# Kernel optimization log

Measured on AMD Instinct MI355X. Metric: run time of the kernel, lower is better.

Reference implementation:

```python
import jax, jax.numpy as jnp
import numpy as np


def _bilinear_sample_zeros(img, px, py):
    """Bilinear sample img [B,C,H,W] at pixel coords px,py [B,...], zeros padding,
    align_corners=True semantics (coords are direct pixel indices)."""
    B, C, H, W = img.shape
    shp = px.shape
    px_f = px.reshape(B, -1)
    py_f = py.reshape(B, -1)
    x0 = jnp.floor(px_f)
    y0 = jnp.floor(py_f)
    fx = px_f - x0  # fractional offsets
    fy = py_f - y0
    x0i = x0.astype(jnp.int32)
    y0i = y0.astype(jnp.int32)
    img_flat = img.reshape(B, C, H * W)

    def corner(xi, yi, w):
        valid = ((xi >= 0) & (xi < W) & (yi >= 0) & (yi < H)).astype(img.dtype)
        xc = jnp.clip(xi, 0, W - 1)
        yc = jnp.clip(yi, 0, H - 1)
        idx = (yc * W + xc)[:, None, :]  # [B,1,N]
        v = jnp.take_along_axis(img_flat, idx, axis=2)  # [B,C,N]
        return v * (w * valid)[:, None, :]

    out = (corner(x0i, y0i, (1.0 - fx) * (1.0 - fy))
           + corner(x0i + 1, y0i, fx * (1.0 - fy))
           + corner(x0i, y0i + 1, (1.0 - fx) * fy)
           + corner(x0i + 1, y0i + 1, fx * fy))
    return out.reshape((B, C) + shp[1:])


def setup_inputs() -> dict:
    key = jax.random.key(0)
    k1, k2, k3 = jax.random.split(key, 3)
    B, C, H, W, D = 2, 32, 128, 256, 48
    x = jax.random.normal(k1, (B, C, H, W), dtype=jnp.float32)
    y = jax.random.normal(k2, (B, C, H, W), dtype=jnp.float32)
    disp = jax.random.uniform(k3, (B, D, H, W), dtype=jnp.float32) * 64.0
    return {"x": x, "y": y, "disp_range_samples": disp, "ndisp": D}


def reference(x, y, disp_range_samples, ndisp):
    B, C, H, W = x.shape
    # pixel coords of the warp: sample right image at (w - disparity, h)
    mw = jnp.arange(W, dtype=x.dtype).reshape(1, 1, 1, W)
    mh = jnp.arange(H, dtype=x.dtype).reshape(1, 1, H, 1)
    px = mw - disp_range_samples                       # [B, D, H, W]
    py = jnp.broadcast_to(mh, px.shape)                # [B, D, H, W]
    warped = _bilinear_sample_zeros(y, px, py)         # [B, C, D, H, W]
    # correlation mode: elementwise multiply with left features, mean over channels
    cost = (warped * x[:, :, None, :, :]).mean(axis=1)  # [B, D, H, W]
    return cost
```

## Files before the change

### kernel.cpp

```cpp
#include <hip/hip_runtime.h>

#define BB 2
#define CC 32
#define HH 128
#define WW 256
#define DD 48
#define HW (HH * WW)
#define NS 65
#define PAD 64
#define YROW (PAD + WW)
#define NT 512


__global__ __launch_bounds__(NT) void cost_volume_kernel(
    const float* __restrict__ x, const float* __restrict__ y,
    const float* __restrict__ disp, float* __restrict__ out) {
  __shared__ float xs[CC * WW];
  __shared__ float ys[CC * YROW];
  __shared__ float corr[NS * WW];

  const int bx = blockIdx.x;
  const int b = bx >> 7;
  const int h = bx & 127;
  const int tid = threadIdx.x;

  const int gbase = (b * CC * HH + h) * WW;
  {
    int c = tid >> 4;
    int j = (tid & 15) << 2;
    *(float4*)&ys[c * YROW + j] = make_float4(0.f, 0.f, 0.f, 0.f);
  }
#pragma unroll
  for (int k = 0; k < 4; ++k) {
    int t = tid + (k << 9);
    int c = t >> 6;
    int w = (t & 63) << 2;
    float4 vx = *(const float4*)(x + gbase + c * HW + w);
    float4 vy = *(const float4*)(y + gbase + c * HW + w);
    *(float4*)&xs[c * WW + w] = vx;
    *(float4*)&ys[c * YROW + PAD + w] = vy;
  }
  __syncthreads();

  const int wid = tid >> 6;
  const int lane = tid & 63;
  const int w0 = lane << 2;
  const int sbase = wid << 3;

  float acc[8][4];
#pragma unroll
  for (int sl = 0; sl < 8; ++sl)
#pragma unroll
    for (int wj = 0; wj < 4; ++wj) acc[sl][wj] = 0.f;
  float a64[4] = {0.f, 0.f, 0.f, 0.f};

  const int A = PAD + w0 - sbase - 8;
#pragma unroll 2
  for (int c = 0; c < CC; ++c) {
    const float* yrow = &ys[c * YROW];
    float4 xv = *(const float4*)&xs[c * WW + w0];
    float4 wv0 = *(const float4*)&yrow[A];
    float4 wv1 = *(const float4*)&yrow[A + 4];
    float4 wv2 = *(const float4*)&yrow[A + 8];
    float win[12] = {wv0.x, wv0.y, wv0.z, wv0.w, wv1.x, wv1.y,
                     wv1.z, wv1.w, wv2.x, wv2.y, wv2.z, wv2.w};
    float xr[4] = {xv.x, xv.y, xv.z, xv.w};
#pragma unroll
    for (int sl = 0; sl < 8; ++sl)
#pragma unroll
      for (int wj = 0; wj < 4; ++wj)
        acc[sl][wj] = fmaf(xr[wj], win[8 + wj - sl], acc[sl][wj]);
    if (wid == 7) {
      float4 yv = *(const float4*)&yrow[w0];
      a64[0] = fmaf(xr[0], yv.x, a64[0]);
      a64[1] = fmaf(xr[1], yv.y, a64[1]);
      a64[2] = fmaf(xr[2], yv.z, a64[2]);
      a64[3] = fmaf(xr[3], yv.w, a64[3]);
    }
  }
#pragma unroll
  for (int sl = 0; sl < 8; ++sl)
    *(float4*)&corr[(sbase + sl) * WW + w0] =
        make_float4(acc[sl][0], acc[sl][1], acc[sl][2], acc[sl][3]);
  if (wid == 7)
    *(float4*)&corr[64 * WW + w0] = make_float4(a64[0], a64[1], a64[2], a64[3]);
  __syncthreads();

  const float inv_c = 1.0f / (float)CC;
  const float* dbase = disp + (b * DD * HH + h) * WW;
  float* obase = out + (b * DD * HH + h) * WW;
#pragma unroll 4
  for (int k = 0; k < (DD * WW) / NT; ++k) {
    int idx = tid + (k << 9);
    int d = idx >> 8;
    int w = idx & 255;
    float dv = dbase[d * HW + w];
    float s0f = ceilf(dv);
    int i0 = (int)s0f;
    float fx = s0f - dv;
    int i1 = (i0 > 0) ? i0 - 1 : 0;
    float c0 = corr[i0 * WW + w];
    float c1 = corr[i1 * WW + w];
    obase[d * HW + w] = (c0 + fx * (c1 - c0)) * inv_c;
  }
}

extern "C" void kernel_launch(void* const* d_in, const int* in_sizes, int n_in,
                              void* d_out, int out_size, void* d_ws, size_t ws_size,
                              hipStream_t stream) {
  const float* x = (const float*)d_in[0];
  const float* y = (const float*)d_in[1];
  const float* disp = (const float*)d_in[2];
  float* out = (float*)d_out;
  cost_volume_kernel<<<BB * HH, NT, 0, stream>>>(x, y, disp, out);
}
```

Measured before the change: 89.55 us.

## Prefetch disparities early, read x directly from global, vectorize output stores

Drops the shared-memory staging of x and has each thread read its x float4 straight from global memory inside the channel loop. Disparity values are prefetched as float4 into registers before the first barrier so their latency overlaps the correlation compute. The output phase now writes float4 stores. This cuts LDS usage and memory stalls in exchange for more register pressure (24 extra floats held live) and global loads inside the hot loop.

```diff
diff --git a/kernel.cpp b/kernel.cpp
--- a/kernel.cpp
+++ b/kernel.cpp
@@ -15,7 +15,6 @@
 __global__ __launch_bounds__(NT) void cost_volume_kernel(
     const float* __restrict__ x, const float* __restrict__ y,
     const float* __restrict__ disp, float* __restrict__ out) {
-  __shared__ float xs[CC * WW];
   __shared__ float ys[CC * YROW];
   __shared__ float corr[NS * WW];
 
@@ -25,6 +24,7 @@
   const int tid = threadIdx.x;
 
   const int gbase = (b * CC * HH + h) * WW;
+
   {
     int c = tid >> 4;
     int j = (tid & 15) << 2;
@@ -35,10 +35,16 @@
     int t = tid + (k << 9);
     int c = t >> 6;
     int w = (t & 63) << 2;
-    float4 vx = *(const float4*)(x + gbase + c * HW + w);
-    float4 vy = *(const float4*)(y + gbase + c * HW + w);
-    *(float4*)&xs[c * WW + w] = vx;
-    *(float4*)&ys[c * YROW + PAD + w] = vy;
+    *(float4*)&ys[c * YROW + PAD + w] = *(const float4*)(y + gbase + c * HW + w);
+  }
+  const float* dbase = disp + (b * DD * HH + h) * WW;
+  float4 dv4[6];
+#pragma unroll
+  for (int j = 0; j < 6; ++j) {
+    int t = tid + (j << 9);
+    int d = t >> 6;
+    int w4 = (t & 63) << 2;
+    dv4[j] = *(const float4*)(dbase + d * HW + w4);
   }
   __syncthreads();
 
@@ -55,10 +61,11 @@
   float a64[4] = {0.f, 0.f, 0.f, 0.f};
 
   const int A = PAD + w0 - sbase - 8;
+  const float* xcol = x + gbase + w0;
 #pragma unroll 2
   for (int c = 0; c < CC; ++c) {
     const float* yrow = &ys[c * YROW];
-    float4 xv = *(const float4*)&xs[c * WW + w0];
+    float4 xv = *(const float4*)(xcol + c * HW);
     float4 wv0 = *(const float4*)&yrow[A];
     float4 wv1 = *(const float4*)&yrow[A + 4];
     float4 wv2 = *(const float4*)&yrow[A + 8];
@@ -87,21 +94,25 @@
   __syncthreads();
 
   const float inv_c = 1.0f / (float)CC;
-  const float* dbase = disp + (b * DD * HH + h) * WW;
   float* obase = out + (b * DD * HH + h) * WW;
-#pragma unroll 4
-  for (int k = 0; k < (DD * WW) / NT; ++k) {
-    int idx = tid + (k << 9);
-    int d = idx >> 8;
-    int w = idx & 255;
-    float dv = dbase[d * HW + w];
-    float s0f = ceilf(dv);
-    int i0 = (int)s0f;
-    float fx = s0f - dv;
-    int i1 = (i0 > 0) ? i0 - 1 : 0;
-    float c0 = corr[i0 * WW + w];
-    float c1 = corr[i1 * WW + w];
-    obase[d * HW + w] = (c0 + fx * (c1 - c0)) * inv_c;
+#pragma unroll
+  for (int j = 0; j < 6; ++j) {
+    int t = tid + (j << 9);
+    int d = t >> 6;
+    int w4 = (t & 63) << 2;
+    float dv[4] = {dv4[j].x, dv4[j].y, dv4[j].z, dv4[j].w};
+    float o[4];
+#pragma unroll
+    for (int e = 0; e < 4; ++e) {
+      float s0f = ceilf(dv[e]);
+      int i0 = (int)s0f;
+      float fx = s0f - dv[e];
+      int i1 = (i0 > 0) ? i0 - 1 : 0;
+      float c0 = corr[i0 * WW + w4 + e];
+      float c1 = corr[i1 * WW + w4 + e];
+      o[e] = (c0 + fx * (c1 - c0)) * inv_c;
+    }
+    *(float4*)(obase + d * HW + w4) = make_float4(o[0], o[1], o[2], o[3]);
   }
 }
 
```

New measurement: 89.23 us. No clear change (-0.4%).
